# Optimization experiments

Hardware: AMD Instinct MI355X
Metric: run time of the kernel (lower is better)

The kernel has to match this reference:

```python
import jax, jax.numpy as jnp
import numpy as np

M = 16
N = 16
T = 100
H1 = (M + N) * 10 * 8          # 2560
H2 = (M * N) * 1 * 4           # 1024
HID = (N * N + M * M) * 10     # 5120, GRU hidden dim


def setup_inputs() -> dict:
    key = jax.random.key(0)
    ks = jax.random.split(key, 16)
    def rn(k, shape, scale=1.0):
        return (jax.random.normal(k, shape, dtype=jnp.float32) * scale)
    inp = {}
    inp["y"] = rn(ks[0], (N, T))
    # scale F so spectral radius ~0.8 -> stable over T steps
    inp["F"] = rn(ks[1], (M, M), 0.2)
    inp["H"] = rn(ks[2], (N, M))
    inp["m1_0"] = rn(ks[3], (M, 1))
    inp["h0"] = rn(ks[4], (HID,))
    D_in, D_out = M + N, M * N
    inp["W1"] = rn(ks[5], (H1, D_in), 1.0 / np.sqrt(D_in))
    inp["b1"] = jnp.zeros((H1,), jnp.float32)
    inp["W_ih"] = rn(ks[6], (3 * HID, H1), 1.0 / np.sqrt(H1))
    inp["b_ih"] = jnp.zeros((3 * HID,), jnp.float32)
    inp["W_hh"] = rn(ks[7], (3 * HID, HID), 1.0 / np.sqrt(HID))
    inp["b_hh"] = jnp.zeros((3 * HID,), jnp.float32)
    inp["W2"] = rn(ks[8], (H2, HID), 1.0 / np.sqrt(HID))
    inp["b2"] = jnp.zeros((H2,), jnp.float32)
    inp["W3"] = rn(ks[9], (D_out, H2), 1.0 / np.sqrt(H2))
    inp["b3"] = jnp.zeros((D_out,), jnp.float32)
    return inp


def _l2_normalize(x):
    # torch F.normalize(p=2, eps=1e-12): x / max(||x||_2, eps)
    return x / jnp.maximum(jnp.linalg.norm(x), 1e-12)


def reference(y, F, H, m1_0, h0, W1, b1, W_ih, b_ih, W_hh, b_hh, W2, b2, W3, b3):
    m, n = F.shape[0], H.shape[0]

    def gru_cell(x, h):
        gi = W_ih @ x + b_ih            # [3*HID]
        gh = W_hh @ h + b_hh            # [3*HID]
        i_r, i_z, i_n = jnp.split(gi, 3)
        h_r, h_z, h_n = jnp.split(gh, 3)
        r = jax.nn.sigmoid(i_r + h_r)
        z = jax.nn.sigmoid(i_z + h_z)
        nn_ = jnp.tanh(i_n + r * h_n)
        return (1.0 - z) * nn_ + z * h

    def step(carry, y_t):
        post, sp_post, h = carry
        # step_prior
        m1x_prior = F @ post            # [m,1]
        m1y = H @ m1x_prior             # [n,1]
        sp_prior = F @ sp_post          # [m,1]
        obs0 = H @ sp_prior             # [n,1]
        # step_KGain_est
        d_norm = _l2_normalize((post - sp_post)[:, 0])
        y_norm = _l2_normalize(y_t - obs0[:, 0])
        kin = jnp.concatenate([d_norm, y_norm])  # [m+n]
        l1 = jax.nn.relu(W1 @ kin + b1)
        h_new = gru_cell(l1, h)
        l2 = jax.nn.relu(W2 @ h_new + b2)
        KG = (W3 @ l2 + b3).reshape(m, n)
        # innovation update
        dy = y_t[:, None] - m1y         # [n,1]
        post_new = m1x_prior + KG @ dy  # [m,1]
        return (post_new, sp_prior, h_new), post_new[:, 0]

    (_, _, _), xs = jax.lax.scan(step, (m1_0, m1_0, h0), y.T)
    return xs.T                         # [m,T]
```

## Files before the change

kernel.cpp:

```cpp
#include <hip/hip_runtime.h>
#include <math.h>

#define Tt  100
#define H1  2560
#define HID 5120
#define H2  1024

typedef float f32x4 __attribute__((ext_vector_type(4)));

enum {
  OFF_POST = 0,
  OFF_SP   = 16,
  OFF_M1X  = 32,
  OFF_M1Y  = 48,
  OFF_SPR  = 64,
  OFF_KIN  = 80,
  OFF_L1   = 112,
  OFF_L2   = 2672,
  OFF_KG   = 3696,
  OFF_HA   = 3952,
  OFF_HB   = 9072,
};

__global__ void k_init(const float* __restrict__ m1_0, const float* __restrict__ h0,
                       float* __restrict__ ws) {
  int i = blockIdx.x * blockDim.x + threadIdx.x;
  if (i < 16) { ws[OFF_POST + i] = m1_0[i]; ws[OFF_SP + i] = m1_0[i]; }
  if (i < HID) ws[OFF_HA + i] = h0[i];
}

__global__ void k_front(const float* __restrict__ Fm, const float* __restrict__ Hm,
                        const float* __restrict__ y, float* __restrict__ ws,
                        float* __restrict__ out,
                        const float* __restrict__ W1, const float* __restrict__ b1,
                        int t, int do_F) {
  __shared__ float s_post[16], s_sp[16], s_m1x[16], s_spr[16], s_d[16], s_yv[16], s_dy[16];
  __shared__ float s_kin[32];
  const int tid = threadIdx.x;
  float* post = ws + OFF_POST;
  float* sp   = ws + OFF_SP;
  float* m1x  = ws + OFF_M1X;
  float* m1y  = ws + OFF_M1Y;
  float* spr  = ws + OFF_SPR;
  const float* KG = ws + OFF_KG;
  const bool w = (blockIdx.x == 0);

  if (do_F) {
    if (tid < 16) s_dy[tid] = y[tid * Tt + (t - 1)] - m1y[tid];
    __syncthreads();
    if (tid < 16) {
      float acc = m1x[tid];
      #pragma unroll
      for (int j = 0; j < 16; j++) acc = fmaf(KG[tid * 16 + j], s_dy[j], acc);
      s_post[tid] = acc;
      float sv = spr[tid];
      s_sp[tid] = sv;
      if (w) { post[tid] = acc; out[tid * Tt + (t - 1)] = acc; sp[tid] = sv; }
    }
    __syncthreads();
  } else {
    if (tid < 16) { s_post[tid] = post[tid]; s_sp[tid] = sp[tid]; }
    __syncthreads();
  }
  if (t >= Tt) return;

  if (tid < 16) {
    float a = 0.f, b = 0.f;
    #pragma unroll
    for (int j = 0; j < 16; j++) {
      a = fmaf(Fm[tid * 16 + j], s_post[j], a);
      b = fmaf(Fm[tid * 16 + j], s_sp[j], b);
    }
    s_m1x[tid] = a; s_spr[tid] = b;
    if (w) { m1x[tid] = a; spr[tid] = b; }
  }
  __syncthreads();
  if (tid < 16) {
    float my = 0.f, ob = 0.f;
    #pragma unroll
    for (int j = 0; j < 16; j++) {
      my = fmaf(Hm[tid * 16 + j], s_m1x[j], my);
      ob = fmaf(Hm[tid * 16 + j], s_spr[j], ob);
    }
    if (w) m1y[tid] = my;
    s_yv[tid] = y[tid * Tt + t] - ob;
    s_d[tid] = s_post[tid] - s_sp[tid];
  }
  __syncthreads();
  if (tid < 16) {
    float nd = 0.f, ny = 0.f;
    #pragma unroll
    for (int j = 0; j < 16; j++) { nd += s_d[j] * s_d[j]; ny += s_yv[j] * s_yv[j]; }
    nd = fmaxf(sqrtf(nd), 1e-12f);
    ny = fmaxf(sqrtf(ny), 1e-12f);
    s_kin[tid]      = s_d[tid] / nd;
    s_kin[16 + tid] = s_yv[tid] / ny;
  }
  __syncthreads();

  const int r = blockIdx.x * 256 + tid;
  const float4* row = (const float4*)(W1 + (size_t)r * 32);
  float acc = b1[r];
  #pragma unroll
  for (int j = 0; j < 8; j++) {
    float4 wv = row[j];
    acc = fmaf(wv.x, s_kin[4 * j + 0], acc);
    acc = fmaf(wv.y, s_kin[4 * j + 1], acc);
    acc = fmaf(wv.z, s_kin[4 * j + 2], acc);
    acc = fmaf(wv.w, s_kin[4 * j + 3], acc);
  }
  ws[OFF_L1 + r] = fmaxf(acc, 0.f);
}

__device__ __forceinline__ float block_reduce_256(float v, float* sdata) {
  const int tid = threadIdx.x;
  #pragma unroll
  for (int off = 32; off > 0; off >>= 1) v += __shfl_down(v, off, 64);
  __syncthreads();
  if ((tid & 63) == 0) sdata[tid >> 6] = v;
  __syncthreads();
  float r = (tid < 4) ? sdata[tid] : 0.f;
  r += __shfl_down(r, 2, 64);
  r += __shfl_down(r, 1, 64);
  return r;
}

__global__ void k_gru(const float* __restrict__ W_ih, const float* __restrict__ b_ih,
                      const float* __restrict__ W_hh, const float* __restrict__ b_hh,
                      const float* __restrict__ l1, const float* __restrict__ h_in,
                      float* __restrict__ h_out) {
  const int i = blockIdx.x;
  const int tid = threadIdx.x;
  __shared__ float sdata[4];
  const float4* l1v = (const float4*)l1;
  const float4* hv  = (const float4*)h_in;
  float p[6];
  #pragma unroll
  for (int g = 0; g < 3; g++) {
    const float4* row = (const float4*)(W_ih + (size_t)(i + g * HID) * H1);
    float acc = 0.f;
    for (int j = tid; j < H1 / 4; j += 256) {
      float4 w = row[j], x = l1v[j];
      acc = fmaf(w.x, x.x, fmaf(w.y, x.y, fmaf(w.z, x.z, fmaf(w.w, x.w, acc))));
    }
    p[g] = acc;
  }
  #pragma unroll
  for (int g = 0; g < 3; g++) {
    const f32x4* row = (const f32x4*)(W_hh + (size_t)(i + g * HID) * HID);
    float acc = 0.f;
    for (int j = tid; j < HID / 4; j += 256) {
      f32x4 w = __builtin_nontemporal_load(row + j);
      float4 x = hv[j];
      acc = fmaf(w.x, x.x, fmaf(w.y, x.y, fmaf(w.z, x.z, fmaf(w.w, x.w, acc))));
    }
    p[3 + g] = acc;
  }
  float s[6];
  #pragma unroll
  for (int k = 0; k < 6; k++) s[k] = block_reduce_256(p[k], sdata);
  if (tid == 0) {
    float ir = s[0] + b_ih[i], iz = s[1] + b_ih[i + HID], inn = s[2] + b_ih[i + 2 * HID];
    float hr = s[3] + b_hh[i], hz = s[4] + b_hh[i + HID], hn  = s[5] + b_hh[i + 2 * HID];
    float r = 1.f / (1.f + expf(-(ir + hr)));
    float z = 1.f / (1.f + expf(-(iz + hz)));
    float nn = tanhf(inn + r * hn);
    h_out[i] = (1.f - z) * nn + z * h_in[i];
  }
}

__global__ void k_l2(const float* __restrict__ W2, const float* __restrict__ b2,
                     const float* __restrict__ h, float* __restrict__ l2) {
  const int j = blockIdx.x;
  const int tid = threadIdx.x;
  __shared__ float sdata[4];
  const float4* row = (const float4*)(W2 + (size_t)j * HID);
  const float4* xv  = (const float4*)h;
  float acc = 0.f;
  for (int k = tid; k < HID / 4; k += 256) {
    float4 w = row[k], x = xv[k];
    acc = fmaf(w.x, x.x, fmaf(w.y, x.y, fmaf(w.z, x.z, fmaf(w.w, x.w, acc))));
  }
  float s = block_reduce_256(acc, sdata);
  if (tid == 0) l2[j] = fmaxf(s + b2[j], 0.f);
}

__global__ void k_kg(const float* __restrict__ W3, const float* __restrict__ b3,
                     const float* __restrict__ l2, float* __restrict__ KG) {
  const int k = blockIdx.x;
  const int tid = threadIdx.x;
  const float4* row = (const float4*)(W3 + (size_t)k * H2);
  const float4* xv  = (const float4*)l2;
  float acc = 0.f;
  for (int j = tid; j < H2 / 4; j += 64) {
    float4 w = row[j], x = xv[j];
    acc = fmaf(w.x, x.x, fmaf(w.y, x.y, fmaf(w.z, x.z, fmaf(w.w, x.w, acc))));
  }
  #pragma unroll
  for (int off = 32; off > 0; off >>= 1) acc += __shfl_down(acc, off, 64);
  if (tid == 0) KG[k] = acc + b3[k];
}

extern "C" void kernel_launch(void* const* d_in, const int* in_sizes, int n_in,
                              void* d_out, int out_size, void* d_ws, size_t ws_size,
                              hipStream_t stream) {
  const float* y    = (const float*)d_in[0];
  const float* Fm   = (const float*)d_in[1];
  const float* Hm   = (const float*)d_in[2];
  const float* m1_0 = (const float*)d_in[3];
  const float* h0   = (const float*)d_in[4];
  const float* W1   = (const float*)d_in[5];
  const float* b1   = (const float*)d_in[6];
  const float* W_ih = (const float*)d_in[7];
  const float* b_ih = (const float*)d_in[8];
  const float* W_hh = (const float*)d_in[9];
  const float* b_hh = (const float*)d_in[10];
  const float* W2   = (const float*)d_in[11];
  const float* b2   = (const float*)d_in[12];
  const float* W3   = (const float*)d_in[13];
  const float* b3   = (const float*)d_in[14];
  float* out = (float*)d_out;
  float* ws  = (float*)d_ws;

  k_init<<<(HID + 255) / 256, 256, 0, stream>>>(m1_0, h0, ws);

  for (int t = 0; t < Tt; t++) {
    k_front<<<H1 / 256, 256, 0, stream>>>(Fm, Hm, y, ws, out, W1, b1, t, t > 0 ? 1 : 0);
    const float* h_in = ws + ((t & 1) ? OFF_HB : OFF_HA);
    float* h_out      = ws + ((t & 1) ? OFF_HA : OFF_HB);
    k_gru<<<HID, 256, 0, stream>>>(W_ih, b_ih, W_hh, b_hh, ws + OFF_L1, h_in, h_out);
    k_l2<<<H2, 256, 0, stream>>>(W2, b2, h_out, ws + OFF_L2);
    k_kg<<<256, 64, 0, stream>>>(W3, b3, ws + OFF_L2, ws + OFF_KG);
  }
  k_front<<<1, 256, 0, stream>>>(Fm, Hm, y, ws, out, W1, b1, Tt, 1);
}
```

Baseline: 9.509 ms.

## Fuse KG projection into front kernel and batch W_hh loads via inline asm

```diff
diff --git a/kernel.cpp b/kernel.cpp
--- a/kernel.cpp
+++ b/kernel.cpp
@@ -33,25 +33,39 @@
                         const float* __restrict__ y, float* __restrict__ ws,
                         float* __restrict__ out,
                         const float* __restrict__ W1, const float* __restrict__ b1,
+                        const float* __restrict__ W3, const float* __restrict__ b3,
                         int t, int do_F) {
   __shared__ float s_post[16], s_sp[16], s_m1x[16], s_spr[16], s_d[16], s_yv[16], s_dy[16];
   __shared__ float s_kin[32];
+  __shared__ float s_KG[256];
   const int tid = threadIdx.x;
   float* post = ws + OFF_POST;
   float* sp   = ws + OFF_SP;
   float* m1x  = ws + OFF_M1X;
   float* m1y  = ws + OFF_M1Y;
   float* spr  = ws + OFF_SPR;
-  const float* KG = ws + OFF_KG;
   const bool w = (blockIdx.x == 0);
 
   if (do_F) {
+    {
+      const float4* row = (const float4*)(W3 + (size_t)tid * H2);
+      const float4* xv  = (const float4*)(ws + OFF_L2);
+      float ax = 0.f, ay = 0.f, az = 0.f, aw = 0.f;
+      for (int j = 0; j < H2 / 4; j++) {
+        float4 wv = row[j], x = xv[j];
+        ax = fmaf(wv.x, x.x, ax);
+        ay = fmaf(wv.y, x.y, ay);
+        az = fmaf(wv.z, x.z, az);
+        aw = fmaf(wv.w, x.w, aw);
+      }
+      s_KG[tid] = ((ax + ay) + az) + aw + b3[tid];
+    }
     if (tid < 16) s_dy[tid] = y[tid * Tt + (t - 1)] - m1y[tid];
     __syncthreads();
     if (tid < 16) {
       float acc = m1x[tid];
       #pragma unroll
-      for (int j = 0; j < 16; j++) acc = fmaf(KG[tid * 16 + j], s_dy[j], acc);
+      for (int j = 0; j < 16; j++) acc = fmaf(s_KG[tid * 16 + j], s_dy[j], acc);
       s_post[tid] = acc;
       float sv = spr[tid];
       s_sp[tid] = sv;
@@ -147,13 +161,31 @@
   }
   #pragma unroll
   for (int g = 0; g < 3; g++) {
-    const f32x4* row = (const f32x4*)(W_hh + (size_t)(i + g * HID) * HID);
+    const float* rowp = W_hh + (size_t)(i + g * HID) * HID;
+    const float* p0 = rowp + 4 * (tid + 0 * 256);
+    const float* p1 = rowp + 4 * (tid + 1 * 256);
+    const float* p2 = rowp + 4 * (tid + 2 * 256);
+    const float* p3 = rowp + 4 * (tid + 3 * 256);
+    const float* p4 = rowp + 4 * (tid + 4 * 256);
+    float4 x0 = hv[tid + 0 * 256];
+    float4 x1 = hv[tid + 1 * 256];
+    float4 x2 = hv[tid + 2 * 256];
+    float4 x3 = hv[tid + 3 * 256];
+    float4 x4 = hv[tid + 4 * 256];
+    f32x4 w0, w1, w2, w3, w4;
+    asm volatile("global_load_dwordx4 %0, %1, off sc1 nt" : "=v"(w0) : "v"(p0));
+    asm volatile("global_load_dwordx4 %0, %1, off sc1 nt" : "=v"(w1) : "v"(p1));
+    asm volatile("global_load_dwordx4 %0, %1, off sc1 nt" : "=v"(w2) : "v"(p2));
+    asm volatile("global_load_dwordx4 %0, %1, off sc1 nt" : "=v"(w3) : "v"(p3));
+    asm volatile("global_load_dwordx4 %0, %1, off sc1 nt" : "=v"(w4) : "v"(p4));
+    asm volatile("s_waitcnt vmcnt(0)" ::: "memory");
+    __builtin_amdgcn_sched_barrier(0);
     float acc = 0.f;
-    for (int j = tid; j < HID / 4; j += 256) {
-      f32x4 w = __builtin_nontemporal_load(row + j);
-      float4 x = hv[j];
-      acc = fmaf(w.x, x.x, fmaf(w.y, x.y, fmaf(w.z, x.z, fmaf(w.w, x.w, acc))));
-    }
+    acc = fmaf(w0.x, x0.x, fmaf(w0.y, x0.y, fmaf(w0.z, x0.z, fmaf(w0.w, x0.w, acc))));
+    acc = fmaf(w1.x, x1.x, fmaf(w1.y, x1.y, fmaf(w1.z, x1.z, fmaf(w1.w, x1.w, acc))));
+    acc = fmaf(w2.x, x2.x, fmaf(w2.y, x2.y, fmaf(w2.z, x2.z, fmaf(w2.w, x2.w, acc))));
+    acc = fmaf(w3.x, x3.x, fmaf(w3.y, x3.y, fmaf(w3.z, x3.z, fmaf(w3.w, x3.w, acc))));
+    acc = fmaf(w4.x, x4.x, fmaf(w4.y, x4.y, fmaf(w4.z, x4.z, fmaf(w4.w, x4.w, acc))));
     p[3 + g] = acc;
   }
   float s[6];
@@ -183,22 +215,6 @@
   }
   float s = block_reduce_256(acc, sdata);
   if (tid == 0) l2[j] = fmaxf(s + b2[j], 0.f);
-}
-
-__global__ void k_kg(const float* __restrict__ W3, const float* __restrict__ b3,
-                     const float* __restrict__ l2, float* __restrict__ KG) {
-  const int k = blockIdx.x;
-  const int tid = threadIdx.x;
-  const float4* row = (const float4*)(W3 + (size_t)k * H2);
-  const float4* xv  = (const float4*)l2;
-  float acc = 0.f;
-  for (int j = tid; j < H2 / 4; j += 64) {
-    float4 w = row[j], x = xv[j];
-    acc = fmaf(w.x, x.x, fmaf(w.y, x.y, fmaf(w.z, x.z, fmaf(w.w, x.w, acc))));
-  }
-  #pragma unroll
-  for (int off = 32; off > 0; off >>= 1) acc += __shfl_down(acc, off, 64);
-  if (tid == 0) KG[k] = acc + b3[k];
 }
 
 extern "C" void kernel_launch(void* const* d_in, const int* in_sizes, int n_in,
@@ -225,12 +241,12 @@
   k_init<<<(HID + 255) / 256, 256, 0, stream>>>(m1_0, h0, ws);
 
   for (int t = 0; t < Tt; t++) {
-    k_front<<<H1 / 256, 256, 0, stream>>>(Fm, Hm, y, ws, out, W1, b1, t, t > 0 ? 1 : 0);
+    k_front<<<H1 / 256, 256, 0, stream>>>(Fm, Hm, y, ws, out, W1, b1, W3, b3,
+                                          t, t > 0 ? 1 : 0);
     const float* h_in = ws + ((t & 1) ? OFF_HB : OFF_HA);
     float* h_out      = ws + ((t & 1) ? OFF_HA : OFF_HB);
     k_gru<<<HID, 256, 0, stream>>>(W_ih, b_ih, W_hh, b_hh, ws + OFF_L1, h_in, h_out);
     k_l2<<<H2, 256, 0, stream>>>(W2, b2, h_out, ws + OFF_L2);
-    k_kg<<<256, 64, 0, stream>>>(W3, b3, ws + OFF_L2, ws + OFF_KG);
-  }
-  k_front<<<1, 256, 0, stream>>>(Fm, Hm, y, ws, out, W1, b1, Tt, 1);
-}
+  }
+  k_front<<<1, 256, 0, stream>>>(Fm, Hm, y, ws, out, W1, b1, W3, b3, Tt, 1);
+}
```

Measured after the change: 11.01 ms. 1.16x slower.

## Transpose W_ih once and skip zero ReLU inputs in a split input-gate matvec

Applied to the files above, without the earlier changes.

```diff
diff --git a/kernel.cpp b/kernel.cpp
--- a/kernel.cpp
+++ b/kernel.cpp
@@ -5,6 +5,10 @@
 #define H1  2560
 #define HID 5120
 #define H2  1024
+#define GI3 (3 * HID)
+#define NJ  64
+#define NR  15
+#define SLICE (H1 / NJ)
 
 typedef float f32x4 __attribute__((ext_vector_type(4)));
 
@@ -20,7 +24,10 @@
   OFF_KG   = 3696,
   OFF_HA   = 3952,
   OFF_HB   = 9072,
+  OFF_GIP  = 14336,
+  OFF_WT   = 997376,
 };
+#define WS_NEED_BYTES ((size_t)(OFF_WT + (size_t)H1 * GI3) * 4)
 
 __global__ void k_init(const float* __restrict__ m1_0, const float* __restrict__ h0,
                        float* __restrict__ ws) {
@@ -29,29 +36,63 @@
   if (i < HID) ws[OFF_HA + i] = h0[i];
 }
 
+#define TS 64
+__global__ void k_tr(const float* __restrict__ A, float* __restrict__ B) {
+  __shared__ float tile[TS][TS + 1];
+  const int jb = blockIdx.x % (H1 / TS);
+  const int rb = blockIdx.x / (H1 / TS);
+  const int tx = threadIdx.x % TS;
+  const int ty0 = threadIdx.x / TS;
+  #pragma unroll
+  for (int k = 0; k < 16; k++) {
+    int ty = ty0 * 16 + k;
+    tile[ty][tx] = A[(size_t)(rb * TS + ty) * H1 + jb * TS + tx];
+  }
+  __syncthreads();
+  #pragma unroll
+  for (int k = 0; k < 16; k++) {
+    int ty = ty0 * 16 + k;
+    B[(size_t)(jb * TS + ty) * GI3 + rb * TS + tx] = tile[tx][ty];
+  }
+}
+
 __global__ void k_front(const float* __restrict__ Fm, const float* __restrict__ Hm,
                         const float* __restrict__ y, float* __restrict__ ws,
                         float* __restrict__ out,
                         const float* __restrict__ W1, const float* __restrict__ b1,
+                        const float* __restrict__ W3, const float* __restrict__ b3,
                         int t, int do_F) {
   __shared__ float s_post[16], s_sp[16], s_m1x[16], s_spr[16], s_d[16], s_yv[16], s_dy[16];
   __shared__ float s_kin[32];
+  __shared__ float s_KG[256];
   const int tid = threadIdx.x;
   float* post = ws + OFF_POST;
   float* sp   = ws + OFF_SP;
   float* m1x  = ws + OFF_M1X;
   float* m1y  = ws + OFF_M1Y;
   float* spr  = ws + OFF_SPR;
-  const float* KG = ws + OFF_KG;
   const bool w = (blockIdx.x == 0);
 
   if (do_F) {
+    {
+      const float4* row = (const float4*)(W3 + (size_t)tid * H2);
+      const float4* xv  = (const float4*)(ws + OFF_L2);
+      float ax = 0.f, ay = 0.f, az = 0.f, aw = 0.f;
+      for (int j = 0; j < H2 / 4; j++) {
+        float4 wv = row[j], x = xv[j];
+        ax = fmaf(wv.x, x.x, ax);
+        ay = fmaf(wv.y, x.y, ay);
+        az = fmaf(wv.z, x.z, az);
+        aw = fmaf(wv.w, x.w, aw);
+      }
+      s_KG[tid] = ((ax + ay) + az) + aw + b3[tid];
+    }
     if (tid < 16) s_dy[tid] = y[tid * Tt + (t - 1)] - m1y[tid];
     __syncthreads();
     if (tid < 16) {
       float acc = m1x[tid];
       #pragma unroll
-      for (int j = 0; j < 16; j++) acc = fmaf(KG[tid * 16 + j], s_dy[j], acc);
+      for (int j = 0; j < 16; j++) acc = fmaf(s_KG[tid * 16 + j], s_dy[j], acc);
       s_post[tid] = acc;
       float sv = spr[tid];
       s_sp[tid] = sv;
@@ -112,6 +153,31 @@
   ws[OFF_L1 + r] = fmaxf(acc, 0.f);
 }
 
+__global__ void k_ih(const float* __restrict__ WT, const float* __restrict__ l1,
+                     float* __restrict__ gip) {
+  const int s  = blockIdx.x / NR;
+  const int rb = blockIdx.x % NR;
+  const int tid = threadIdx.x;
+  __shared__ float sl1[SLICE];
+  if (tid < SLICE) sl1[tid] = l1[s * SLICE + tid];
+  __syncthreads();
+  const f32x4* WT4 = (const f32x4*)WT;
+  const int col = rb * 256 + tid;
+  f32x4 acc = {0.f, 0.f, 0.f, 0.f};
+  #pragma unroll 4
+  for (int k = 0; k < SLICE; k++) {
+    float lv = sl1[k];
+    if (lv != 0.f) {
+      f32x4 wv = WT4[(size_t)(s * SLICE + k) * (GI3 / 4) + col];
+      acc.x = fmaf(lv, wv.x, acc.x);
+      acc.y = fmaf(lv, wv.y, acc.y);
+      acc.z = fmaf(lv, wv.z, acc.z);
+      acc.w = fmaf(lv, wv.w, acc.w);
+    }
+  }
+  ((f32x4*)gip)[(size_t)s * (GI3 / 4) + col] = acc;
+}
+
 __device__ __forceinline__ float block_reduce_256(float v, float* sdata) {
   const int tid = threadIdx.x;
   #pragma unroll
@@ -125,15 +191,58 @@
   return r;
 }
 
-__global__ void k_gru(const float* __restrict__ W_ih, const float* __restrict__ b_ih,
-                      const float* __restrict__ W_hh, const float* __restrict__ b_hh,
-                      const float* __restrict__ l1, const float* __restrict__ h_in,
-                      float* __restrict__ h_out) {
+__global__ void k_gru2(const float* __restrict__ gip,
+                       const float* __restrict__ b_ih,
+                       const float* __restrict__ W_hh, const float* __restrict__ b_hh,
+                       const float* __restrict__ h_in, float* __restrict__ h_out) {
+  const int i = blockIdx.x;
+  const int tid = threadIdx.x;
+  __shared__ float sdata[4];
+  __shared__ float s_gi[3];
+  if (tid < 64) {
+    #pragma unroll
+    for (int g = 0; g < 3; g++) {
+      float v = gip[(size_t)tid * GI3 + g * HID + i];
+      #pragma unroll
+      for (int off = 32; off > 0; off >>= 1) v += __shfl_down(v, off, 64);
+      if (tid == 0) s_gi[g] = v;
+    }
+  }
+  const f32x4* hv = (const f32x4*)h_in;
+  float p[3];
+  #pragma unroll
+  for (int g = 0; g < 3; g++) {
+    const f32x4* row = (const f32x4*)(W_hh + (size_t)(i + g * HID) * HID);
+    float acc = 0.f;
+    for (int j = tid; j < HID / 4; j += 256) {
+      f32x4 w = __builtin_nontemporal_load(row + j);
+      f32x4 x = hv[j];
+      acc = fmaf(w.x, x.x, fmaf(w.y, x.y, fmaf(w.z, x.z, fmaf(w.w, x.w, acc))));
+    }
+    p[g] = acc;
+  }
+  float s[3];
+  #pragma unroll
+  for (int k = 0; k < 3; k++) s[k] = block_reduce_256(p[k], sdata);
+  if (tid == 0) {
+    float ir = s_gi[0] + b_ih[i], iz = s_gi[1] + b_ih[i + HID], inn = s_gi[2] + b_ih[i + 2 * HID];
+    float hr = s[0] + b_hh[i],   hz = s[1] + b_hh[i + HID],    hn  = s[2] + b_hh[i + 2 * HID];
+    float r = 1.f / (1.f + expf(-(ir + hr)));
+    float z = 1.f / (1.f + expf(-(iz + hz)));
+    float nn = tanhf(inn + r * hn);
+    h_out[i] = (1.f - z) * nn + z * h_in[i];
+  }
+}
+
+__global__ void k_gru_dense(const float* __restrict__ W_ih, const float* __restrict__ b_ih,
+                            const float* __restrict__ W_hh, const float* __restrict__ b_hh,
+                            const float* __restrict__ l1, const float* __restrict__ h_in,
+                            float* __restrict__ h_out) {
   const int i = blockIdx.x;
   const int tid = threadIdx.x;
   __shared__ float sdata[4];
   const float4* l1v = (const float4*)l1;
-  const float4* hv  = (const float4*)h_in;
+  const f32x4* hv  = (const f32x4*)h_in;
   float p[6];
   #pragma unroll
   for (int g = 0; g < 3; g++) {
@@ -151,7 +260,7 @@
     float acc = 0.f;
     for (int j = tid; j < HID / 4; j += 256) {
       f32x4 w = __builtin_nontemporal_load(row + j);
-      float4 x = hv[j];
+      f32x4 x = hv[j];
       acc = fmaf(w.x, x.x, fmaf(w.y, x.y, fmaf(w.z, x.z, fmaf(w.w, x.w, acc))));
     }
     p[3 + g] = acc;
@@ -183,22 +292,6 @@
   }
   float s = block_reduce_256(acc, sdata);
   if (tid == 0) l2[j] = fmaxf(s + b2[j], 0.f);
-}
-
-__global__ void k_kg(const float* __restrict__ W3, const float* __restrict__ b3,
-                     const float* __restrict__ l2, float* __restrict__ KG) {
-  const int k = blockIdx.x;
-  const int tid = threadIdx.x;
-  const float4* row = (const float4*)(W3 + (size_t)k * H2);
-  const float4* xv  = (const float4*)l2;
-  float acc = 0.f;
-  for (int j = tid; j < H2 / 4; j += 64) {
-    float4 w = row[j], x = xv[j];
-    acc = fmaf(w.x, x.x, fmaf(w.y, x.y, fmaf(w.z, x.z, fmaf(w.w, x.w, acc))));
-  }
-  #pragma unroll
-  for (int off = 32; off > 0; off >>= 1) acc += __shfl_down(acc, off, 64);
-  if (tid == 0) KG[k] = acc + b3[k];
 }
 
 extern "C" void kernel_launch(void* const* d_in, const int* in_sizes, int n_in,
@@ -222,15 +315,25 @@
   float* out = (float*)d_out;
   float* ws  = (float*)d_ws;
 
+  const bool sparse = (ws_size >= WS_NEED_BYTES);
+
   k_init<<<(HID + 255) / 256, 256, 0, stream>>>(m1_0, h0, ws);
+  if (sparse) {
+    k_tr<<<(H1 / TS) * (GI3 / TS), 256, 0, stream>>>(W_ih, ws + OFF_WT);
+  }
 
   for (int t = 0; t < Tt; t++) {
-    k_front<<<H1 / 256, 256, 0, stream>>>(Fm, Hm, y, ws, out, W1, b1, t, t > 0 ? 1 : 0);
+    k_front<<<H1 / 256, 256, 0, stream>>>(Fm, Hm, y, ws, out, W1, b1, W3, b3,
+                                          t, t > 0 ? 1 : 0);
     const float* h_in = ws + ((t & 1) ? OFF_HB : OFF_HA);
     float* h_out      = ws + ((t & 1) ? OFF_HA : OFF_HB);
-    k_gru<<<HID, 256, 0, stream>>>(W_ih, b_ih, W_hh, b_hh, ws + OFF_L1, h_in, h_out);
+    if (sparse) {
+      k_ih<<<NJ * NR, 256, 0, stream>>>(ws + OFF_WT, ws + OFF_L1, ws + OFF_GIP);
+      k_gru2<<<HID, 256, 0, stream>>>(ws + OFF_GIP, b_ih, W_hh, b_hh, h_in, h_out);
+    } else {
+      k_gru_dense<<<HID, 256, 0, stream>>>(W_ih, b_ih, W_hh, b_hh, ws + OFF_L1, h_in, h_out);
+    }
     k_l2<<<H2, 256, 0, stream>>>(W2, b2, h_out, ws + OFF_L2);
-    k_kg<<<256, 64, 0, stream>>>(W3, b3, ws + OFF_L2, ws + OFF_KG);
-  }
-  k_front<<<1, 256, 0, stream>>>(Fm, Hm, y, ws, out, W1, b1, Tt, 1);
-}
+  }
+  k_front<<<1, 256, 0, stream>>>(Fm, Hm, y, ws, out, W1, b1, W3, b3, Tt, 1);
+}
```

New measurement: 12.04 ms. 26.6% more time.
